# Optimization experiments

Measured on AMD Instinct MI355X. Metric: run time of the kernel, lower is better.

Reference implementation:

```python
import jax, jax.numpy as jnp
import numpy as np


def setup_inputs() -> dict:
    key = jax.random.key(0)
    k1, k2, k3, k4 = jax.random.split(key, 4)
    B, L, H, E = 2, 10000, 8, 64
    NE = 160000
    return {
        "queries": jax.random.normal(k1, (B, L, H, E), dtype=jnp.float32),
        "keys": jax.random.normal(k2, (B, L, H, E), dtype=jnp.float32),
        "values": jax.random.normal(k3, (B, L, H, E), dtype=jnp.float32),
        "adj": jax.random.randint(k4, (2, NE), 0, L, dtype=jnp.int64),
    }


def reference(queries, keys, values, adj):
    # queries/keys/values: [B, L, H, E]; adj: [2, NE] (row 0 = dst group, row 1 = src)
    B, L, H, E = queries.shape
    softmax_temp = 1.0 / (E ** 0.5)
    dst = adj[0]
    src = adj[1]

    # edge-gather dot product: qk[b, e, h] = sum_d q[b, dst[e], h, d] * k[b, src[e], h, d]
    qk = jnp.sum(queries[:, dst] * keys[:, src], axis=-1) * softmax_temp  # [B, NE, H]

    # segment softmax grouped by destination node (dropout is identity at eval)
    qk_e = qk.transpose(1, 0, 2)  # [NE, B, H] (segment ops act on leading axis)
    seg_max = jax.ops.segment_max(qk_e, dst, num_segments=L)  # [L, B, H]
    ex = jnp.exp(qk_e - seg_max[dst])
    seg_sum = jax.ops.segment_sum(ex, dst, num_segments=L)  # [L, B, H]
    alpha = ex / (seg_sum[dst] + 1e-16)  # [NE, B, H]

    # spmm: gather v at src, weight by alpha, scatter-add to dst
    weighted = values[:, src] * alpha.transpose(1, 0, 2)[..., None]  # [B, NE, H, E]
    out = jnp.zeros_like(values).at[:, dst].add(weighted)  # [B, L, H, E]
    return out
```

## Files before the change

### kernel.cpp

```cpp
#include <hip/hip_runtime.h>

#define BB 2
#define HH 8
#define EE 64
#define ROW (HH * EE)
#define HC 4

typedef float vf4 __attribute__((ext_vector_type(4)));

__device__ inline unsigned short f2bf(float f) {
  unsigned int u = __float_as_uint(f);
  u = (u + 0x7fffu + ((u >> 16) & 1u)) >> 16;
  return (unsigned short)u;
}

__global__ __launch_bounds__(256) void convert_hist_kernel(
    const float* __restrict__ k, const float* __restrict__ v,
    unsigned short* __restrict__ kbf, unsigned short* __restrict__ vbf,
    const int* __restrict__ dst, int* __restrict__ counts,
    int n4, int NE) {
  int i = blockIdx.x * blockDim.x + threadIdx.x;
  if (i < n4) {
    vf4 kf = __builtin_nontemporal_load((const vf4*)k + i);
    vf4 vf = __builtin_nontemporal_load((const vf4*)v + i);
    ((ushort4*)kbf)[i] = make_ushort4(f2bf(kf.x), f2bf(kf.y), f2bf(kf.z), f2bf(kf.w));
    ((ushort4*)vbf)[i] = make_ushort4(f2bf(vf.x), f2bf(vf.y), f2bf(vf.z), f2bf(vf.w));
  }
  if (i < NE) {
    atomicAdd(&counts[dst[i]], 1);
  }
}

__global__ __launch_bounds__(1024) void scan_kernel(
    const int* __restrict__ counts_in, int* __restrict__ counts_mut,
    int* __restrict__ offsets, int L) {
  __shared__ int sums[1024];
  int tid = threadIdx.x;
  int chunk = (L + 1023) / 1024;
  int beg = tid * chunk;
  int end = min(beg + chunk, L);
  int s = 0;
  for (int i = beg; i < end; ++i) s += counts_in[i];
  sums[tid] = s;
  __syncthreads();
  for (int off = 1; off < 1024; off <<= 1) {
    int val = 0;
    if (tid >= off) val = sums[tid - off];
    __syncthreads();
    if (tid >= off) sums[tid] += val;
    __syncthreads();
  }
  int run = (tid > 0) ? sums[tid - 1] : 0;
  for (int i = beg; i < end; ++i) {
    offsets[i] = run;
    run += counts_in[i];
    counts_mut[i] = 0;
  }
  if (tid == 1023) offsets[L] = run;
}

__global__ __launch_bounds__(256) void fill_csr_kernel(
    const int* __restrict__ dst, const int* __restrict__ src,
    const int* __restrict__ offsets, int* __restrict__ cursor,
    int* __restrict__ csr_src, int NE) {
  int e = blockIdx.x * blockDim.x + threadIdx.x;
  if (e >= NE) return;
  int d = dst[e];
  int pos = atomicAdd(&cursor[d], 1);
  csr_src[offsets[d] + pos] = src[e];
}

__device__ inline void bf8_unpack(uint4 u, float* f) {
  f[0] = __uint_as_float(u.x << 16);
  f[1] = __uint_as_float(u.x & 0xffff0000u);
  f[2] = __uint_as_float(u.y << 16);
  f[3] = __uint_as_float(u.y & 0xffff0000u);
  f[4] = __uint_as_float(u.z << 16);
  f[5] = __uint_as_float(u.z & 0xffff0000u);
  f[6] = __uint_as_float(u.w << 16);
  f[7] = __uint_as_float(u.w & 0xffff0000u);
}

#define LOAD_HC(KK, VV, TT, CNT)                                      \
  _Pragma("unroll") for (int i_ = 0; i_ < HC; ++i_) {                 \
    if (i_ < (CNT)) {                                                 \
      int s_ = csr_src[(TT) + i_];                                    \
      KK[i_] = kb_base[(size_t)s_ * (ROW / 8) + lane];                \
      VV[i_] = vb_base[(size_t)s_ * (ROW / 8) + lane];                \
    }                                                                 \
  }

#define COMPUTE_HC(KK, VV, CNT)                                       \
  do {                                                                \
    float qk_[HC];                                                    \
    float cmax_ = -INFINITY;                                          \
    _Pragma("unroll") for (int i_ = 0; i_ < HC; ++i_) {               \
      if (i_ < (CNT)) {                                               \
        float kf_[8];                                                 \
        bf8_unpack(KK[i_], kf_);                                      \
        float p_ = q0.x * kf_[0] + q0.y * kf_[1] + q0.z * kf_[2] +    \
                   q0.w * kf_[3] + q1.x * kf_[4] + q1.y * kf_[5] +    \
                   q1.z * kf_[6] + q1.w * kf_[7];                     \
        p_ += __shfl_xor(p_, 1);                                      \
        p_ += __shfl_xor(p_, 2);                                      \
        p_ += __shfl_xor(p_, 4);                                      \
        qk_[i_] = p_;                                                 \
        cmax_ = fmaxf(cmax_, p_);                                     \
      }                                                               \
    }                                                                 \
    if (__any(cmax_ > m)) {        \
      float mnew_ = fmaxf(m, cmax_);                                  \
      float scale_ = __expf(m - mnew_); \
      l_run *= scale_;                                                \
      _Pragma("unroll") for (int j_ = 0; j_ < 8; ++j_) acc[j_] *= scale_; \
      m = mnew_;                                                      \
    }                                                                 \
    _Pragma("unroll") for (int i_ = 0; i_ < HC; ++i_) {               \
      if (i_ < (CNT)) {                                               \
        float a_ = __expf(qk_[i_] - m);                               \
        l_run += a_;                                                  \
        float vfv_[8];                                                \
        bf8_unpack(VV[i_], vfv_);                                     \
        _Pragma("unroll") for (int j_ = 0; j_ < 8; ++j_)              \
            acc[j_] += a_ * vfv_[j_];                                 \
      }                                                               \
    }                                                                 \
  } while (0)

__global__ __launch_bounds__(256) void fused_attn_kernel(
    const float* __restrict__ q, const unsigned short* __restrict__ kbf,
    const unsigned short* __restrict__ vbf, const int* __restrict__ offsets,
    const int* __restrict__ csr_src, float* __restrict__ out, int L) {
  int wid = blockIdx.x * (blockDim.x >> 6) + (threadIdx.x >> 6);
  int lane = threadIdx.x & 63;
  if (wid >= L * BB) return;
  int d = wid >> 1;
  int b = wid & 1;
  int beg = offsets[d];
  int end = offsets[d + 1];

  const vf4* qrow = (const vf4*)(q + ((size_t)b * L + d) * ROW);
  vf4 q0 = __builtin_nontemporal_load(qrow + lane * 2 + 0);
  vf4 q1 = __builtin_nontemporal_load(qrow + lane * 2 + 1);
  q0 *= 0.125f;
  q1 *= 0.125f;

  float m = -INFINITY;
  float l_run = 0.0f;
  float acc[8];
#pragma unroll
  for (int i = 0; i < 8; ++i) acc[i] = 0.0f;

  const uint4* kb_base = (const uint4*)(kbf + (size_t)b * L * ROW);
  const uint4* vb_base = (const uint4*)(vbf + (size_t)b * L * ROW);

  uint4 kA[HC], vA[HC], kB[HC], vB[HC];
  int t = beg;
  int cntA = min(HC, end - t);
  LOAD_HC(kA, vA, t, cntA);
  t += cntA;
  int cntB = min(HC, end - t);
  LOAD_HC(kB, vB, t, cntB);
  t += cntB;

  for (;;) {
    if (cntA <= 0) break;
    COMPUTE_HC(kA, vA, cntA);
    cntA = min(HC, end - t);
    LOAD_HC(kA, vA, t, cntA);
    t += cntA;
    if (cntB <= 0) break;
    COMPUTE_HC(kB, vB, cntB);
    cntB = min(HC, end - t);
    LOAD_HC(kB, vB, t, cntB);
    t += cntB;
  }

  float r = 1.0f / (l_run + 1e-16f);
  vf4* orow = (vf4*)(out + ((size_t)b * L + d) * ROW);
  vf4 o0 = {acc[0] * r, acc[1] * r, acc[2] * r, acc[3] * r};
  vf4 o1 = {acc[4] * r, acc[5] * r, acc[6] * r, acc[7] * r};
  __builtin_nontemporal_store(o0, orow + lane * 2 + 0);
  __builtin_nontemporal_store(o1, orow + lane * 2 + 1);
}

extern "C" void kernel_launch(void* const* d_in, const int* in_sizes, int n_in,
                              void* d_out, int out_size, void* d_ws, size_t ws_size,
                              hipStream_t stream) {
  const float* q = (const float*)d_in[0];
  const float* k = (const float*)d_in[1];
  const float* v = (const float*)d_in[2];
  const int* adj = (const int*)d_in[3];

  const int NE = in_sizes[3] / 2;
  const int L = in_sizes[0] / (BB * HH * EE);
  const int* dst = adj;
  const int* src = adj + NE;
  const int nelem = BB * L * HH * EE;

  char* ws = (char*)d_ws;
  size_t off = 0;
  unsigned short* kbf = (unsigned short*)(ws + off); off += (size_t)nelem * 2;
  unsigned short* vbf = (unsigned short*)(ws + off); off += (size_t)nelem * 2;
  int* counts = (int*)(ws + off);   off += (size_t)L * 4;
  int* offsets = (int*)(ws + off);  off += (size_t)(L + 1) * 4;
  int* csr_src = (int*)(ws + off);  off += (size_t)NE * 4;

  hipMemsetAsync(counts, 0, (size_t)L * 4, stream);

  int n4 = nelem / 4;
  convert_hist_kernel<<<(n4 + 255) / 256, 256, 0, stream>>>(
      k, v, kbf, vbf, dst, counts, n4, NE);

  scan_kernel<<<1, 1024, 0, stream>>>(counts, counts, offsets, L);

  fill_csr_kernel<<<(NE + 255) / 256, 256, 0, stream>>>(
      dst, src, offsets, counts, csr_src, NE);

  int nwaves = L * BB;
  fused_attn_kernel<<<(nwaves + 3) / 4, 256, 0, stream>>>(
      q, kbf, vbf, offsets, csr_src, (float*)d_out, L);
}
```

Baseline: 286.6 us.

## Fuse CSR preprocessing into one cooperative kernel with grid-wide syncs

The memset, bf16 conversion plus histogram, the single-block scan and the CSR fill are merged into one cooperative kernel of 1024 blocks that uses grid.sync between phases. The scan becomes a two-level parallel scan: per-block scans, then a scan of the block sums in block 0. This removes several kernel launches and the serial single-block scan, at the cost of five grid barriers and a fixed grid size. The index math in the K/V gather also switches from 64-bit to 32-bit unsigned to save address arithmetic.

```diff
diff --git a/kernel.cpp b/kernel.cpp
--- a/kernel.cpp
+++ b/kernel.cpp
@@ -1,4 +1,7 @@
 #include <hip/hip_runtime.h>
+#include <hip/hip_cooperative_groups.h>
+
+namespace cg = cooperative_groups;
 
 #define BB 2
 #define HH 8
@@ -6,6 +9,9 @@
 #define ROW (HH * EE)
 #define HC 4
 
+#define PREP_NB 1024
+#define PREP_BS 256
+
 typedef float vf4 __attribute__((ext_vector_type(4)));
 
 __device__ inline unsigned short f2bf(float f) {
@@ -14,60 +20,89 @@
   return (unsigned short)u;
 }
 
-__global__ __launch_bounds__(256) void convert_hist_kernel(
+__global__ __launch_bounds__(PREP_BS) void prep_kernel(
     const float* __restrict__ k, const float* __restrict__ v,
     unsigned short* __restrict__ kbf, unsigned short* __restrict__ vbf,
-    const int* __restrict__ dst, int* __restrict__ counts,
-    int n4, int NE) {
-  int i = blockIdx.x * blockDim.x + threadIdx.x;
-  if (i < n4) {
+    const int* __restrict__ dst, const int* __restrict__ src,
+    int* __restrict__ counts, int* __restrict__ offsets,
+    int* __restrict__ blocksum, int* __restrict__ csr_src,
+    int n4, int NE, int L) {
+  cg::grid_group grid = cg::this_grid();
+  __shared__ int sh[PREP_BS];
+  const int tid = threadIdx.x;
+  const int gid = blockIdx.x * PREP_BS + tid;
+  const int T = gridDim.x * PREP_BS;
+
+  for (int i = gid; i < L; i += T) counts[i] = 0;
+  grid.sync();
+
+  for (int i = gid; i < n4; i += T) {
     vf4 kf = __builtin_nontemporal_load((const vf4*)k + i);
     vf4 vf = __builtin_nontemporal_load((const vf4*)v + i);
     ((ushort4*)kbf)[i] = make_ushort4(f2bf(kf.x), f2bf(kf.y), f2bf(kf.z), f2bf(kf.w));
     ((ushort4*)vbf)[i] = make_ushort4(f2bf(vf.x), f2bf(vf.y), f2bf(vf.z), f2bf(vf.w));
   }
-  if (i < NE) {
-    atomicAdd(&counts[dst[i]], 1);
-  }
-}
-
-__global__ __launch_bounds__(1024) void scan_kernel(
-    const int* __restrict__ counts_in, int* __restrict__ counts_mut,
-    int* __restrict__ offsets, int L) {
-  __shared__ int sums[1024];
-  int tid = threadIdx.x;
-  int chunk = (L + 1023) / 1024;
-  int beg = tid * chunk;
-  int end = min(beg + chunk, L);
-  int s = 0;
-  for (int i = beg; i < end; ++i) s += counts_in[i];
-  sums[tid] = s;
+  for (int i = gid; i < NE; i += T) atomicAdd(&counts[dst[i]], 1);
+  grid.sync();
+
+  const int nbl = (L + PREP_BS - 1) / PREP_BS;
+  const int node = gid;
+  int c = (node < L) ? counts[node] : 0;
+  sh[tid] = c;
   __syncthreads();
-  for (int off = 1; off < 1024; off <<= 1) {
-    int val = 0;
-    if (tid >= off) val = sums[tid - off];
-    __syncthreads();
-    if (tid >= off) sums[tid] += val;
-    __syncthreads();
-  }
-  int run = (tid > 0) ? sums[tid - 1] : 0;
-  for (int i = beg; i < end; ++i) {
-    offsets[i] = run;
-    run += counts_in[i];
-    counts_mut[i] = 0;
-  }
-  if (tid == 1023) offsets[L] = run;
-}
-
-__global__ __launch_bounds__(256) void fill_csr_kernel(
-    const int* __restrict__ dst, const int* __restrict__ src,
-    const int* __restrict__ offsets, int* __restrict__ cursor,
-    int* __restrict__ csr_src, int NE) {
-  int e = blockIdx.x * blockDim.x + threadIdx.x;
-  if (e >= NE) return;
-  int d = dst[e];
-  int pos = atomicAdd(&cursor[d], 1);
-  csr_src[offsets[d] + pos] = src[e];
+#pragma unroll
+  for (int off = 1; off < PREP_BS; off <<= 1) {
+    int t2 = (tid >= off) ? sh[tid - off] : 0;
+    __syncthreads();
+    sh[tid] += t2;
+    __syncthreads();
+  }
+  if (node < L) offsets[node] = sh[tid] - c;
+  if (tid == PREP_BS - 1 && blockIdx.x < nbl) blocksum[blockIdx.x] = sh[tid];
+  grid.sync();
+
+  if (blockIdx.x == 0) {
+    int base_i = tid * 4;
+    int vloc[4];
+    int s = 0;
+#pragma unroll
+    for (int u = 0; u < 4; ++u) {
+      int idx = base_i + u;
+      vloc[u] = (idx < nbl) ? blocksum[idx] : 0;
+      s += vloc[u];
+    }
+    __syncthreads();
+    sh[tid] = s;
+    __syncthreads();
+#pragma unroll
+    for (int off = 1; off < PREP_BS; off <<= 1) {
+      int t2 = (tid >= off) ? sh[tid - off] : 0;
+      __syncthreads();
+      sh[tid] += t2;
+      __syncthreads();
+    }
+    int ebase = sh[tid] - s;
+#pragma unroll
+    for (int u = 0; u < 4; ++u) {
+      int idx = base_i + u;
+      if (idx < nbl) blocksum[idx] = ebase;
+      ebase += vloc[u];
+    }
+    if (tid == PREP_BS - 1) offsets[L] = sh[tid];
+  }
+  grid.sync();
+
+  if (node < L) {
+    offsets[node] += blocksum[node >> 8];
+    counts[node] = 0;
+  }
+  grid.sync();
+
+  for (int e = gid; e < NE; e += T) {
+    int d = dst[e];
+    int pos = atomicAdd(&counts[d], 1);
+    csr_src[offsets[d] + pos] = src[e];
+  }
 }
 
 __device__ inline void bf8_unpack(uint4 u, float* f) {
@@ -84,9 +119,9 @@
 #define LOAD_HC(KK, VV, TT, CNT)                                      \
   _Pragma("unroll") for (int i_ = 0; i_ < HC; ++i_) {                 \
     if (i_ < (CNT)) {                                                 \
-      int s_ = csr_src[(TT) + i_];                                    \
-      KK[i_] = kb_base[(size_t)s_ * (ROW / 8) + lane];                \
-      VV[i_] = vb_base[(size_t)s_ * (ROW / 8) + lane];                \
+      unsigned s_ = (unsigned)csr_src[(TT) + i_];                     \
+      KK[i_] = kb_base[s_ * (unsigned)(ROW / 8) + lane];              \
+      VV[i_] = vb_base[s_ * (unsigned)(ROW / 8) + lane];              \
     }                                                                 \
   }
 
@@ -205,17 +240,16 @@
   int* counts = (int*)(ws + off);   off += (size_t)L * 4;
   int* offsets = (int*)(ws + off);  off += (size_t)(L + 1) * 4;
   int* csr_src = (int*)(ws + off);  off += (size_t)NE * 4;
-
-  hipMemsetAsync(counts, 0, (size_t)L * 4, stream);
+  int* blocksum = (int*)(ws + off); off += (size_t)PREP_NB * 4;
 
   int n4 = nelem / 4;
-  convert_hist_kernel<<<(n4 + 255) / 256, 256, 0, stream>>>(
-      k, v, kbf, vbf, dst, counts, n4, NE);
-
-  scan_kernel<<<1, 1024, 0, stream>>>(counts, counts, offsets, L);
-
-  fill_csr_kernel<<<(NE + 255) / 256, 256, 0, stream>>>(
-      dst, src, offsets, counts, csr_src, NE);
+
+  void* args[] = {
+      (void*)&k, (void*)&v, (void*)&kbf, (void*)&vbf,
+      (void*)&dst, (void*)&src, (void*)&counts, (void*)&offsets,
+      (void*)&blocksum, (void*)&csr_src, (void*)&n4, (void*)&NE, (void*)&L};
+  hipLaunchCooperativeKernel((void*)prep_kernel, dim3(PREP_NB), dim3(PREP_BS),
+                             args, 0, stream);
 
   int nwaves = L * BB;
   fused_attn_kernel<<<(nwaves + 3) / 4, 256, 0, stream>>>(
```

Measured after the change: 747.8 us. +161.0%, slower.
